# Kernel optimization log

Measured on AMD Instinct MI355X. Metric: run time of the kernel, lower is better.

The kernel has to match this reference:

```python
import jax, jax.numpy as jnp
import numpy as np

# module config (matches init_kwargs)
H, W, C = 32, 32, 3
KH, KW, KC = 4, 4, 1
N_CLASS = 10
NBIN = 200
SHIFT = (0, 0)
NH, NW, NC = H // KH, W // KW, C // KC
NKERNEL = NH * NW * NC          # 192
NDIM_SUB = KH * KW * KC         # 16
NCOMP = NDIM_SUB                # n_component defaults to ndim_sub
NDIM = H * W * C                # 3072
NTRANS = NKERNEL * NCOMP        # 3072
N = 2048


def setup_inputs() -> dict:
    key = jax.random.key(0)
    k1, k2, k3, k4, k5, k6 = jax.random.split(key, 6)
    data = jax.random.normal(k1, (N, NDIM), dtype=jnp.float32)
    label = jax.random.randint(k2, (N,), 0, N_CLASS)
    # per-patch orthonormal projections: QR with sign fix, as in __init__
    wi = jax.random.normal(k3, (NKERNEL, NDIM_SUB, NCOMP), dtype=jnp.float32)
    Q, R = jnp.linalg.qr(wi)
    sign = jnp.sign(jnp.diagonal(R, axis1=-2, axis2=-1))
    wT_blocks = Q * sign[:, None, :]
    # monotone rational-quadratic spline knots per class / transformed dim
    dx = jax.random.uniform(k4, (N_CLASS, NTRANS, NBIN - 1), minval=0.5, maxval=1.5)
    dy = jax.random.uniform(k5, (N_CLASS, NTRANS, NBIN - 1), minval=0.5, maxval=1.5)
    z = jnp.zeros((N_CLASS, NTRANS, 1), jnp.float32)
    knots_x = -4.0 + 8.0 * jnp.concatenate([z, jnp.cumsum(dx, -1)], -1) / jnp.sum(dx, -1, keepdims=True)
    knots_y = -4.0 + 8.0 * jnp.concatenate([z, jnp.cumsum(dy, -1)], -1) / jnp.sum(dy, -1, keepdims=True)
    knots_d = jax.random.uniform(k6, (N_CLASS, NTRANS, NBIN), minval=0.5, maxval=1.5)
    return {"data": data, "label": label, "wT_blocks": wT_blocks,
            "knots_x": knots_x.astype(jnp.float32), "knots_y": knots_y.astype(jnp.float32),
            "knots_d": knots_d}


def construct_wT(wT_blocks):
    """Assemble block-structured (NDIM, NTRANS) projection from per-patch blocks."""
    dim = jnp.arange(NDIM).reshape(H, W, C)
    dim = jnp.roll(dim, (-SHIFT[0], -SHIFT[1]), axis=(0, 1))  # Shift() == negative roll
    # rows[b] = flat pixel indices of patch b; block order index = h*NW*NC + w*NC + c
    rows = dim.reshape(NH, KH, NW, KW, C).transpose(0, 2, 4, 1, 3).reshape(NKERNEL, NDIM_SUB)
    cols = jnp.arange(NKERNEL)[:, None] * NCOMP + jnp.arange(NCOMP)[None, :]
    wT = jnp.zeros((NDIM, NTRANS), wT_blocks.dtype)
    return wT.at[rows[:, :, None], cols[:, None, :]].set(wT_blocks)


def rq_spline(x, xx, yy, dd):
    """Monotone rational-quadratic spline with linear extrapolation.
    x: (N, T); xx/yy/dd: (T, K) knot positions / values / derivatives.
    Returns (y, log|dy/dx|), each (N, T)."""
    xT = x.T  # (T, N)
    lo, hi = xx[:, :1], xx[:, -1:]
    below, above = xT < lo, xT > hi
    xc = jnp.clip(xT, lo, hi)  # keep interior branch NaN-free
    k = jax.vmap(lambda kn, v: jnp.searchsorted(kn, v, side='right'))(xx, xc) - 1
    k = jnp.clip(k, 0, NBIN - 2)
    take = lambda a, i: jnp.take_along_axis(a, i, axis=1)
    xk, xk1 = take(xx, k), take(xx, k + 1)
    yk, yk1 = take(yy, k), take(yy, k + 1)
    dk, dk1 = take(dd, k), take(dd, k + 1)
    wdt = xk1 - xk
    s = (yk1 - yk) / wdt
    xi = (xc - xk) / wdt
    om = 1.0 - xi
    denom = s + (dk1 + dk - 2.0 * s) * xi * om
    ys = yk + (yk1 - yk) * (s * xi * xi + dk * xi * om) / denom
    lj_s = 2.0 * jnp.log(s) + jnp.log(dk1 * xi * xi + 2.0 * s * xi * om + dk * om * om) - 2.0 * jnp.log(denom)
    d0, dK = dd[:, :1], dd[:, -1:]
    y = jnp.where(below, yy[:, :1] + (xT - lo) * d0,
                  jnp.where(above, yy[:, -1:] + (xT - hi) * dK, ys))
    lj = jnp.where(below, jnp.log(d0), jnp.where(above, jnp.log(dK), lj_s))
    return y.T, lj.T


def reference(data, label, wT_blocks, knots_x, knots_y, knots_d):
    wT = construct_wT(wT_blocks)                 # (NDIM, NTRANS)
    data0 = data @ wT                            # (N, NTRANS)
    remaining = data - data0 @ wT.T              # orthogonal complement (zero here since full-rank)

    def body(carry, params):
        c, data1, logj = carry
        xx, yy, dd = params
        y, lj = rq_spline(data0, xx, yy, dd)
        m = label == c
        data1 = jnp.where(m[:, None], y, data1)
        logj = jnp.where(m, jnp.sum(lj, axis=1), logj)
        return (c + 1, data1, logj), None

    init = (jnp.int32(0), jnp.zeros_like(data0), jnp.zeros((data.shape[0],), data.dtype))
    (_, data1, logj), _ = jax.lax.scan(body, init, (knots_x, knots_y, knots_d))
    out = remaining + data1 @ wT.T
    return out, logj
```

## Files before the change

### kernel.cpp

```cpp
#include <hip/hip_runtime.h>

constexpr int NSAMP  = 2048;
constexpr int NDIM   = 3072;
constexpr int NTRANS = 3072;
constexpr int NBIN   = 200;
constexpr int NCLASS = 10;
constexpr int NPATCH = 192;
constexpr int BLK    = 256;
constexpr int PER_T  = NDIM / BLK;
constexpr int DSTR   = 20;
constexpr int SA     = 4;
constexpr int SC     = 4;
constexpr int NL     = 128;
constexpr int LUTS   = 136;

__device__ __forceinline__ float4* xb_line(float* xb, int p, int sl) {
    return (float4*)(xb + ((size_t)p * NSAMP + (sl ^ (p & 63))) * 16);
}
__device__ __forceinline__ const float4* xb_line_c(const float* xb, int p, int sl) {
    return (const float4*)(xb + ((size_t)p * NSAMP + (sl ^ (p & 63))) * 16);
}

__global__ __launch_bounds__(1024)
void p0_prep(const int* __restrict__ label,
             int* __restrict__ slot,
             int* __restrict__ cls_off,
             float* __restrict__ logj_slot)
{
    __shared__ int s_lab[NSAMP];
    __shared__ int s_cnt[32][NCLASS];
    __shared__ int s_pre[32][NCLASS];
    __shared__ int s_tot[NCLASS];
    __shared__ int s_off[NCLASS + 1];
    const int tid  = threadIdx.x;
    const int lane = tid & 63;
    const int wv   = tid >> 6;

    for (int i = tid; i < NSAMP; i += 1024) {
        s_lab[i] = label[i];
        logj_slot[i] = 0.f;
    }
    __syncthreads();

    const unsigned long long ltmask = ((unsigned long long)1 << lane) - 1;
    int myrank[2], myc[2];
    #pragma unroll
    for (int pass = 0; pass < 2; ++pass) {
        const int n = pass * 1024 + tid;
        const int c = s_lab[n];
        myc[pass] = c;
        int r = 0;
        #pragma unroll
        for (int cls = 0; cls < NCLASS; ++cls) {
            const unsigned long long b = __ballot(c == cls);
            if (lane == 0) s_cnt[pass * 16 + wv][cls] = __popcll(b);
            if (cls == c)  r = __popcll(b & ltmask);
        }
        myrank[pass] = r;
    }
    __syncthreads();

    if (tid < 32 * NCLASS) {
        const int seg = tid & 31;
        const int cls = tid >> 5;
        int acc = 0;
        for (int s = 0; s < seg; ++s) acc += s_cnt[s][cls];
        s_pre[seg][cls] = acc;
        if (seg == 31) s_tot[cls] = acc + s_cnt[31][cls];
    }
    __syncthreads();
    if (tid == 0) {
        int a = 0;
        for (int c = 0; c < NCLASS; ++c) { s_off[c] = a; a += s_tot[c]; }
        s_off[NCLASS] = a;
    }
    __syncthreads();

    #pragma unroll
    for (int pass = 0; pass < 2; ++pass) {
        const int n   = pass * 1024 + tid;
        const int seg = pass * 16 + wv;
        const int c   = myc[pass];
        slot[n] = s_off[c] + s_pre[seg][c] + myrank[pass];
    }
    if (tid <= NCLASS) cls_off[tid] = s_off[tid];
}

__global__ __launch_bounds__(BLK, 4)
void pA_project(const float* __restrict__ data,
                const float* __restrict__ B,
                const int*   __restrict__ slot,
                float* __restrict__ xb)
{
    __shared__ float s_data[SA][NDIM];
    const int b   = blockIdx.x;
    const int tid = threadIdx.x;
    const int n0  = b * SA;

    #pragma unroll
    for (int s = 0; s < SA; ++s) {
        const float4* dr = (const float4*)(data + (size_t)(n0 + s) * NDIM);
        float4* sd = (float4*)s_data[s];
        #pragma unroll
        for (int j = 0; j < 3; ++j)
            sd[tid + BLK * j] = dr[tid + BLK * j];
    }
    int sls[SA];
    #pragma unroll
    for (int s = 0; s < SA; ++s) sls[s] = slot[n0 + s];
    __syncthreads();

    #pragma unroll 1
    for (int jj = 0; jj < 3; ++jj) {
        const int tau = tid + BLK * jj;
        const int p   = tau >> 2;
        const int q4  = tau & 3;
        const int nh  = p / 24;
        const int rem = p - nh * 24;
        const int nw  = rem / 3;
        const int ch  = rem - nw * 3;
        const int rowbase = nh * 384 + nw * 12 + ch;

        float4 Bp[16];
        const float4* Bg = (const float4*)(B + p * 256 + q4 * 4);
        #pragma unroll
        for (int i = 0; i < 16; ++i) Bp[i] = Bg[i * 4];

        #pragma unroll
        for (int s = 0; s < SA; ++s) {
            float dv[16];
            #pragma unroll
            for (int i = 0; i < 16; ++i)
                dv[i] = s_data[s][rowbase + (i >> 2) * 96 + (i & 3) * 3];

            float acc[4] = {0.f, 0.f, 0.f, 0.f};
            #pragma unroll
            for (int i = 0; i < 16; ++i) {
                acc[0] += Bp[i].x * dv[i];
                acc[1] += Bp[i].y * dv[i];
                acc[2] += Bp[i].z * dv[i];
                acc[3] += Bp[i].w * dv[i];
            }
            *(xb_line(xb, p, sls[s]) + q4) =
                make_float4(acc[0], acc[1], acc[2], acc[3]);
        }
    }
}

__global__ __launch_bounds__(BLK, 4)
void pB_spline(const float* __restrict__ kx,
               const float* __restrict__ ky,
               const float* __restrict__ kd,
               const int*   __restrict__ cls_off,
               float* __restrict__ xb,
               float* __restrict__ logj_slot)
{
    __shared__ float s_kx[16 * NBIN];
    __shared__ float s_kyd[16 * NBIN * 2];
    __shared__ unsigned char s_lut[16 * LUTS];

    const int p   = blockIdx.x;
    const int c   = blockIdx.y;
    const int tid = threadIdx.x;
    const int t0  = p * 16;

    const size_t kofs = ((size_t)c * NTRANS + t0) * NBIN;
    const float4* gx = (const float4*)(kx + kofs);
    const float4* gy = (const float4*)(ky + kofs);
    const float4* gd = (const float4*)(kd + kofs);
    float4* lx = (float4*)s_kx;
    #pragma unroll 1
    for (int i = tid; i < 16 * NBIN / 4; i += BLK) {
        lx[i] = gx[i];
        const float4 vy = gy[i];
        const float4 vd = gd[i];
        const int base = i * 8;
        s_kyd[base + 0] = vy.x; s_kyd[base + 1] = vd.x;
        s_kyd[base + 2] = vy.y; s_kyd[base + 3] = vd.y;
        s_kyd[base + 4] = vy.z; s_kyd[base + 5] = vd.z;
        s_kyd[base + 6] = vy.w; s_kyd[base + 7] = vd.w;
    }
    __syncthreads();

    {
        const int r  = tid >> 4;
        const int ch = tid & 15;
        const float* xx = s_kx + r * NBIN;
        const int j0 = ch * 8;
        const float xu0 = -4.0f + (float)j0 * (8.0f / NL);
        int klo = 0, khi = NBIN;
        #pragma unroll
        for (int it = 0; it < 8; ++it) {
            const int mid = (klo + khi) >> 1;
            const bool le = (xx[mid] <= xu0);
            klo = le ? mid : klo;
            khi = le ? khi : mid;
        }
        int k = klo;
        const int nj = (ch == 15) ? 9 : 8;
        unsigned char* lrow = s_lut + r * LUTS + j0;
        #pragma unroll 1
        for (int jj = 0; jj < nj; ++jj) {
            const float xuj = -4.0f + (float)(j0 + jj) * (8.0f / NL);
            while (k < NBIN - 1 && xx[k + 1] <= xuj) ++k;
            lrow[jj] = (unsigned char)k;
        }
    }
    __syncthreads();

    const int qq  = tid & 3;
    const int sid = tid >> 2;
    const float* sxx = s_kx + qq * 4 * NBIN;

    const int beg = cls_off[c];
    const int end = cls_off[c + 1];
    const int nit = (end - beg + 63) >> 6;

    int sl = beg + sid;
    float4 v = make_float4(0.f, 0.f, 0.f, 0.f);
    float4* lcur = nullptr;
    if (sl < end) { lcur = xb_line(xb, p, sl) + qq; v = *lcur; }

    #pragma unroll 1
    for (int it = 0; it < nit; ++it) {
        const int sln = sl + 64;
        float4 vn = make_float4(0.f, 0.f, 0.f, 0.f);
        float4* lnx = nullptr;
        if (it + 1 < nit && sln < end) { lnx = xb_line(xb, p, sln) + qq; vn = *lnx; }

        if (lcur) {
            float xs[4] = {v.x, v.y, v.z, v.w};
            float lj_sum = 0.f;
            #pragma unroll
            for (int j = 0; j < 4; ++j) {
                const float* xx  = sxx + j * NBIN;
                const float* yd  = s_kyd + (qq * 4 + j) * (NBIN * 2);
                const unsigned char* lrow = s_lut + (qq * 4 + j) * LUTS;
                const float x  = xs[j];
                const float lo = xx[0];
                const float hi = xx[NBIN - 1];

                float y, lj;
                if (x < lo) {
                    const float d0 = yd[1];
                    y  = yd[0] + (x - lo) * d0;
                    lj = __logf(d0);
                } else if (x > hi) {
                    const float dK = yd[(NBIN - 1) * 2 + 1];
                    y  = yd[(NBIN - 1) * 2] + (x - hi) * dK;
                    lj = __logf(dK);
                } else {
                    int u = (int)((x + 4.0f) * (NL / 8.0f));
                    u = u < 0 ? 0 : (u > NL - 1 ? NL - 1 : u);
                    int klo = (int)lrow[u] - 1;
                    klo = klo < 0 ? 0 : klo;
                    int khi = (int)lrow[u + 1] + 2;
                    khi = khi > NBIN ? NBIN : khi;
                    #pragma unroll
                    for (int itb = 0; itb < 3; ++itb) {
                        const int mid = (klo + khi) >> 1;
                        const bool le = (xx[mid] <= x);
                        klo = le ? mid : klo;
                        khi = le ? khi : mid;
                    }
                    int k = klo;
                    if (k > NBIN - 2) k = NBIN - 2;

                    const float xk = xx[k], xk1 = xx[k + 1];
                    const float2 p0 = *(const float2*)&yd[k * 2];
                    const float2 p1 = *(const float2*)&yd[k * 2 + 2];
                    const float yk = p0.x, dk = p0.y;
                    const float yk1 = p1.x, dk1 = p1.y;

                    const float wdt     = xk1 - xk;
                    const float inv_wdt = __fdividef(1.f, wdt);
                    const float dy      = yk1 - yk;
                    const float s       = dy * inv_wdt;
                    const float xi      = (x - xk) * inv_wdt;
                    const float om      = 1.f - xi;
                    const float denom   = s + (dk1 + dk - 2.f * s) * xi * om;
                    const float r       = __fdividef(1.f, denom);
                    const float num     = dy * (s * xi * xi + dk * xi * om);
                    y = yk + num * r;
                    const float Nq = dk1 * xi * xi + 2.f * s * xi * om + dk * om * om;
                    const float t2 = s * r;
                    lj = __logf(t2 * t2 * Nq);
                }
                xs[j] = y - x;
                lj_sum += lj;
            }

            *lcur = make_float4(xs[0], xs[1], xs[2], xs[3]);

            lj_sum += __shfl_xor(lj_sum, 1);
            lj_sum += __shfl_xor(lj_sum, 2);
            if (qq == 0) atomicAdd(&logj_slot[sl], lj_sum);
        }

        sl = sln; lcur = lnx; v = vn;
    }
}

__global__ __launch_bounds__(BLK, 2)
void pC_recon(const float* __restrict__ data,
              const float* __restrict__ B,
              const int*   __restrict__ slot,
              const float* __restrict__ xb,
              const float* __restrict__ logj_slot,
              float* __restrict__ out,
              float* __restrict__ logj)
{
    __shared__ float s_diff[SC][NPATCH * DSTR];
    const int b   = blockIdx.x;
    const int tid = threadIdx.x;
    const int n0  = b * SC;

    #pragma unroll
    for (int s = 0; s < SC; ++s) {
        const int sl = slot[n0 + s];
        #pragma unroll
        for (int jj = 0; jj < 3; ++jj) {
            const int i  = tid + BLK * jj;
            const int pp = i >> 2;
            const int q  = i & 3;
            const float4 v = *(xb_line_c(xb, pp, sl) + q);
            *(float4*)&s_diff[s][pp * DSTR + q * 4] = v;
        }
    }
    if (tid < SC) logj[n0 + tid] = logj_slot[slot[n0 + tid]];
    __syncthreads();

    #pragma unroll 1
    for (int j = 0; j < PER_T; ++j) {
        const int d  = tid + BLK * j;
        const int ch = d % 3;
        const int hw = d / 3;
        const int w  = hw & 31;
        const int h  = hw >> 5;
        const int p  = ((h >> 2) * 8 + (w >> 2)) * 3 + ch;
        const int i  = (h & 3) * 4 + (w & 3);

        const float4* Bp4 = (const float4*)(B + p * 256 + i * 16);
        const float4 b0 = Bp4[0], b1 = Bp4[1], b2 = Bp4[2], b3 = Bp4[3];

        #pragma unroll
        for (int s = 0; s < SC; ++s) {
            const float4* dp4 = (const float4*)&s_diff[s][p * DSTR];
            const float4 d0 = dp4[0], d1 = dp4[1], d2 = dp4[2], d3 = dp4[3];
            float acc = data[(size_t)(n0 + s) * NDIM + d];
            acc += b0.x * d0.x + b0.y * d0.y + b0.z * d0.z + b0.w * d0.w;
            acc += b1.x * d1.x + b1.y * d1.y + b1.z * d1.z + b1.w * d1.w;
            acc += b2.x * d2.x + b2.y * d2.y + b2.z * d2.z + b2.w * d2.w;
            acc += b3.x * d3.x + b3.y * d3.y + b3.z * d3.z + b3.w * d3.w;
            out[(size_t)(n0 + s) * NDIM + d] = acc;
        }
    }
}

extern "C" void kernel_launch(void* const* d_in, const int* in_sizes, int n_in,
                              void* d_out, int out_size, void* d_ws, size_t ws_size,
                              hipStream_t stream) {
    const float* data  = (const float*)d_in[0];
    const int*   label = (const int*)  d_in[1];
    const float* B     = (const float*)d_in[2];
    const float* kx    = (const float*)d_in[3];
    const float* ky    = (const float*)d_in[4];
    const float* kd    = (const float*)d_in[5];

    float* out  = (float*)d_out;
    float* logj = (float*)d_out + (size_t)NSAMP * NDIM;

    char* ws = (char*)d_ws;
    size_t off = 0;
    float* xb        = (float*)(ws + off); off += (size_t)NPATCH * NSAMP * 16 * 4;
    float* logj_slot = (float*)(ws + off); off += NSAMP * 4;
    int*   slot      = (int*)  (ws + off); off += NSAMP * 4;
    int*   cls_off   = (int*)  (ws + off); off += 64;

    p0_prep   <<<1, 1024, 0, stream>>>(label, slot, cls_off, logj_slot);
    pA_project<<<NSAMP / SA, BLK, 0, stream>>>(data, B, slot, xb);
    dim3 gridB(NPATCH, NCLASS);
    pB_spline <<<gridB, BLK, 0, stream>>>(kx, ky, kd, cls_off, xb, logj_slot);
    pC_recon  <<<NSAMP / SC, BLK, 0, stream>>>(data, B, slot, xb, logj_slot, out, logj);
}
```

Baseline: 203.7 us.

## Split spline blocks by dim-half, use finer lookup table with fixed-window search

```diff
diff --git a/kernel.cpp b/kernel.cpp
--- a/kernel.cpp
+++ b/kernel.cpp
@@ -10,9 +10,9 @@
 constexpr int PER_T  = NDIM / BLK;
 constexpr int DSTR   = 20;
 constexpr int SA     = 4;
-constexpr int SC     = 4;
-constexpr int NL     = 128;
-constexpr int LUTS   = 136;
+constexpr int SC     = 2;
+constexpr int NL     = 1024;
+constexpr int LUTS   = 1024;
 
 __device__ __forceinline__ float4* xb_line(float* xb, int p, int sl) {
     return (float4*)(xb + ((size_t)p * NSAMP + (sl ^ (p & 63))) * 16);
@@ -147,7 +147,7 @@
     }
 }
 
-__global__ __launch_bounds__(BLK, 4)
+__global__ __launch_bounds__(BLK, 5)
 void pB_spline(const float* __restrict__ kx,
                const float* __restrict__ ky,
                const float* __restrict__ kd,
@@ -155,14 +155,15 @@
                float* __restrict__ xb,
                float* __restrict__ logj_slot)
 {
-    __shared__ float s_kx[16 * NBIN];
-    __shared__ float s_kyd[16 * NBIN * 2];
-    __shared__ unsigned char s_lut[16 * LUTS];
-
-    const int p   = blockIdx.x;
-    const int c   = blockIdx.y;
-    const int tid = threadIdx.x;
-    const int t0  = p * 16;
+    __shared__ float s_kx[8 * NBIN];
+    __shared__ float s_kyd[8 * NBIN * 2];
+    __shared__ unsigned char s_lut[8 * LUTS];
+
+    const int p    = blockIdx.x;
+    const int c    = blockIdx.y;
+    const int half = blockIdx.z;
+    const int tid  = threadIdx.x;
+    const int t0   = p * 16 + half * 8;
 
     const size_t kofs = ((size_t)c * NTRANS + t0) * NBIN;
     const float4* gx = (const float4*)(kx + kofs);
@@ -170,7 +171,7 @@
     const float4* gd = (const float4*)(kd + kofs);
     float4* lx = (float4*)s_kx;
     #pragma unroll 1
-    for (int i = tid; i < 16 * NBIN / 4; i += BLK) {
+    for (int i = tid; i < 8 * NBIN / 4; i += BLK) {
         lx[i] = gx[i];
         const float4 vy = gy[i];
         const float4 vd = gd[i];
@@ -183,10 +184,10 @@
     __syncthreads();
 
     {
-        const int r  = tid >> 4;
-        const int ch = tid & 15;
-        const float* xx = s_kx + r * NBIN;
-        const int j0 = ch * 8;
+        const int lr = tid >> 5;
+        const int ch = tid & 31;
+        const float* xx = s_kx + lr * NBIN;
+        const int j0 = ch * 32;
         const float xu0 = -4.0f + (float)j0 * (8.0f / NL);
         int klo = 0, khi = NBIN;
         #pragma unroll
@@ -197,10 +198,9 @@
             khi = le ? khi : mid;
         }
         int k = klo;
-        const int nj = (ch == 15) ? 9 : 8;
-        unsigned char* lrow = s_lut + r * LUTS + j0;
+        unsigned char* lrow = s_lut + lr * LUTS + j0;
         #pragma unroll 1
-        for (int jj = 0; jj < nj; ++jj) {
+        for (int jj = 0; jj < 32; ++jj) {
             const float xuj = -4.0f + (float)(j0 + jj) * (8.0f / NL);
             while (k < NBIN - 1 && xx[k + 1] <= xuj) ++k;
             lrow[jj] = (unsigned char)k;
@@ -208,37 +208,44 @@
     }
     __syncthreads();
 
-    const int qq  = tid & 3;
-    const int sid = tid >> 2;
+    const int qq  = tid & 1;
+    const int sid = tid >> 1;
     const float* sxx = s_kx + qq * 4 * NBIN;
+
+    float lo_r[4], hi_r[4];
+    #pragma unroll
+    for (int j = 0; j < 4; ++j) {
+        lo_r[j] = sxx[j * NBIN];
+        hi_r[j] = sxx[j * NBIN + NBIN - 1];
+    }
 
     const int beg = cls_off[c];
     const int end = cls_off[c + 1];
-    const int nit = (end - beg + 63) >> 6;
+    const int nit = (end - beg + 127) >> 7;
 
     int sl = beg + sid;
     float4 v = make_float4(0.f, 0.f, 0.f, 0.f);
     float4* lcur = nullptr;
-    if (sl < end) { lcur = xb_line(xb, p, sl) + qq; v = *lcur; }
+    if (sl < end) { lcur = xb_line(xb, p, sl) + half * 2 + qq; v = *lcur; }
 
     #pragma unroll 1
     for (int it = 0; it < nit; ++it) {
-        const int sln = sl + 64;
+        const int sln = sl + 128;
         float4 vn = make_float4(0.f, 0.f, 0.f, 0.f);
         float4* lnx = nullptr;
-        if (it + 1 < nit && sln < end) { lnx = xb_line(xb, p, sln) + qq; vn = *lnx; }
+        if (it + 1 < nit && sln < end) { lnx = xb_line(xb, p, sln) + half * 2 + qq; vn = *lnx; }
 
         if (lcur) {
             float xs[4] = {v.x, v.y, v.z, v.w};
             float lj_sum = 0.f;
             #pragma unroll
             for (int j = 0; j < 4; ++j) {
-                const float* xx  = sxx + j * NBIN;
-                const float* yd  = s_kyd + (qq * 4 + j) * (NBIN * 2);
+                const float* xx = sxx + j * NBIN;
+                const float* yd = s_kyd + (qq * 4 + j) * (NBIN * 2);
                 const unsigned char* lrow = s_lut + (qq * 4 + j) * LUTS;
                 const float x  = xs[j];
-                const float lo = xx[0];
-                const float hi = xx[NBIN - 1];
+                const float lo = lo_r[j];
+                const float hi = hi_r[j];
 
                 float y, lj;
                 if (x < lo) {
@@ -253,20 +260,21 @@
                     int u = (int)((x + 4.0f) * (NL / 8.0f));
                     u = u < 0 ? 0 : (u > NL - 1 ? NL - 1 : u);
                     int klo = (int)lrow[u] - 1;
-                    klo = klo < 0 ? 0 : klo;
-                    int khi = (int)lrow[u + 1] + 2;
-                    khi = khi > NBIN ? NBIN : khi;
-                    #pragma unroll
-                    for (int itb = 0; itb < 3; ++itb) {
-                        const int mid = (klo + khi) >> 1;
-                        const bool le = (xx[mid] <= x);
-                        klo = le ? mid : klo;
-                        khi = le ? khi : mid;
-                    }
-                    int k = klo;
-                    if (k > NBIN - 2) k = NBIN - 2;
-
-                    const float xk = xx[k], xk1 = xx[k + 1];
+                    klo = klo < 0 ? 0 : (klo > NBIN - 6 ? NBIN - 6 : klo);
+                    const float v0 = xx[klo];
+                    const float v1 = xx[klo + 1];
+                    const float v2 = xx[klo + 2];
+                    const float v3 = xx[klo + 3];
+                    const float v4 = xx[klo + 4];
+                    const float v5 = xx[klo + 5];
+                    const int cnt = (int)(v1 <= x) + (int)(v2 <= x)
+                                  + (int)(v3 <= x) + (int)(v4 <= x);
+                    const int k = klo + cnt;
+                    const float xk  = cnt == 0 ? v0 : cnt == 1 ? v1 :
+                                      cnt == 2 ? v2 : cnt == 3 ? v3 : v4;
+                    const float xk1 = cnt == 0 ? v1 : cnt == 1 ? v2 :
+                                      cnt == 2 ? v3 : cnt == 3 ? v4 : v5;
+
                     const float2 p0 = *(const float2*)&yd[k * 2];
                     const float2 p1 = *(const float2*)&yd[k * 2 + 2];
                     const float yk = p0.x, dk = p0.y;
@@ -293,7 +301,6 @@
             *lcur = make_float4(xs[0], xs[1], xs[2], xs[3]);
 
             lj_sum += __shfl_xor(lj_sum, 1);
-            lj_sum += __shfl_xor(lj_sum, 2);
             if (qq == 0) atomicAdd(&logj_slot[sl], lj_sum);
         }
 
@@ -301,7 +308,7 @@
     }
 }
 
-__global__ __launch_bounds__(BLK, 2)
+__global__ __launch_bounds__(BLK, 5)
 void pC_recon(const float* __restrict__ data,
               const float* __restrict__ B,
               const int*   __restrict__ slot,
@@ -379,7 +386,7 @@
 
     p0_prep   <<<1, 1024, 0, stream>>>(label, slot, cls_off, logj_slot);
     pA_project<<<NSAMP / SA, BLK, 0, stream>>>(data, B, slot, xb);
-    dim3 gridB(NPATCH, NCLASS);
+    dim3 gridB(NPATCH, NCLASS, 2);
     pB_spline <<<gridB, BLK, 0, stream>>>(kx, ky, kd, cls_off, xb, logj_slot);
     pC_recon  <<<NSAMP / SC, BLK, 0, stream>>>(data, B, slot, xb, logj_slot, out, logj);
 }
```

Result: slower. 224.5 us (+10.2%).
